# Kernel tuning notes

Measured on AMD Instinct MI355X. Metric: run time of the kernel, lower is better.

The kernel has to match this reference:

```python
import jax, jax.numpy as jnp
import numpy as np

N_NODES = 20000
N_EDGES = 320000
IN_CH = 512
HEADS = 4
OUT_CH = 128
NEG_SLOPE = 0.2  # PyG GATConv default leaky_relu slope


def setup_inputs() -> dict:
    key = jax.random.key(0)
    k1, k2, k3, k4, k5 = jax.random.split(key, 5)
    x = jax.random.normal(k1, (N_NODES, IN_CH), dtype=jnp.float32)
    edge_index = jax.random.randint(k2, (2, N_EDGES), 0, N_NODES, dtype=jnp.int64)
    # Learned parameters (glorot-ish scaling)
    W = jax.random.normal(k3, (IN_CH, HEADS * OUT_CH), dtype=jnp.float32) * np.float32(1.0 / np.sqrt(IN_CH))
    att_src = jax.random.normal(k4, (HEADS, OUT_CH), dtype=jnp.float32) * np.float32(0.1)
    att_dst = jax.random.normal(k5, (HEADS, OUT_CH), dtype=jnp.float32) * np.float32(0.1)
    bias = jnp.zeros((OUT_CH,), dtype=jnp.float32)
    return {"x": x, "W": W, "att_src": att_src, "att_dst": att_dst, "bias": bias, "edge_index": edge_index}


def reference(x, W, att_src, att_dst, bias, edge_index):
    N = x.shape[0]
    H, C = att_src.shape
    # add self-loops (PyG GATConv default add_self_loops=True)
    loop = jnp.arange(N, dtype=edge_index.dtype)
    ei = jnp.concatenate([edge_index, jnp.stack([loop, loop])], axis=1)
    src, dst = ei[0], ei[1]
    # linear projection: [N, H, C]
    xl = (x @ W).reshape(N, H, C)
    # per-node attention halves: [N, H]
    a_s = jnp.einsum('nhc,hc->nh', xl, att_src)
    a_d = jnp.einsum('nhc,hc->nh', xl, att_dst)
    # per-edge logits + segment softmax over incoming edges (grouped by dst)
    alpha = jax.nn.leaky_relu(a_s[src] + a_d[dst], negative_slope=NEG_SLOPE)  # [E, H]
    amax = jax.ops.segment_max(alpha, dst, num_segments=N)  # every node has a self-loop -> no empty segments
    ae = jnp.exp(alpha - amax[dst])
    denom = jax.ops.segment_sum(ae, dst, num_segments=N)
    alpha = ae / (denom[dst] + 1e-16)
    # weighted scatter-add of source features: [N, H, C]
    out = jax.ops.segment_sum(alpha[:, :, None] * xl[src], dst, num_segments=N)
    # concat=False -> mean over heads, then bias [C]
    out = out.mean(axis=1) + bias
    return jax.nn.elu(out)
```

## Files before the change

### kernel.cpp

```cpp
#include <hip/hip_runtime.h>
#include <math.h>

#define N_NODES 20000
#define N_PAD 20096
#define N_EDGES 320000
#define IN_CH 512
#define HEADS 4
#define OUT_CH 128
#define HC 512
#define NEG_SLOPE 0.2f

#define CVX_BLOCKS 5024
#define CVW_BLOCKS 64
#define CNT_BLOCKS 1250

#define GEMM_WGS 628
#define GEMM_XQ 78
#define GEMM_XR 4

typedef __attribute__((ext_vector_type(8))) short short8;
typedef __attribute__((ext_vector_type(4))) float float4v;

__device__ __forceinline__ int detect_is64(const int* __restrict__ ei32) {
    int is64 = 1;
    #pragma unroll
    for (int i = 0; i < 32; i++) is64 &= (ei32[2 * i + 1] == 0);
    return is64;
}

__device__ __forceinline__ int edge_at(const void* ei, int is64, long long idx) {
    return is64 ? (int)((const long long*)ei)[idx] : ((const int*)ei)[idx];
}

__device__ __forceinline__ unsigned short f2bf(float f) {
    union { float f; unsigned u; } v; v.f = f;
    unsigned r = v.u + 0x7fffu + ((v.u >> 16) & 1u);
    return (unsigned short)(r >> 16);
}

__device__ __forceinline__ void bf8_decode(uint4 r, float* f) {
    f[0] = __uint_as_float(r.x << 16); f[1] = __uint_as_float(r.x & 0xffff0000u);
    f[2] = __uint_as_float(r.y << 16); f[3] = __uint_as_float(r.y & 0xffff0000u);
    f[4] = __uint_as_float(r.z << 16); f[5] = __uint_as_float(r.z & 0xffff0000u);
    f[6] = __uint_as_float(r.w << 16); f[7] = __uint_as_float(r.w & 0xffff0000u);
}

__device__ __forceinline__ float leaky(float t) { return t > 0.f ? t : NEG_SLOPE * t; }

__device__ __forceinline__ float sel_head(float4 w, int hd) {
    float lo = (hd & 1) ? w.y : w.x;
    float hi = (hd & 1) ? w.w : w.z;
    return (hd & 2) ? hi : lo;
}

__global__ __launch_bounds__(256) void fusedA_kernel(const float* __restrict__ x,
                                                     const float* __restrict__ W,
                                                     unsigned short* __restrict__ xb,
                                                     unsigned short* __restrict__ Wt,
                                                     const void* __restrict__ ei,
                                                     int* __restrict__ counts,
                                                     int* __restrict__ epos) {
    __shared__ float tile[64][65];
    int b = blockIdx.x;
    if (b < CVX_BLOCKS) {
        size_t i = ((size_t)b * 256 + threadIdx.x) * 8;
        unsigned short o[8];
        if (i < (size_t)N_NODES * IN_CH) {
            float4 f0 = *(const float4*)&x[i];
            float4 f1 = *(const float4*)&x[i + 4];
            o[0] = f2bf(f0.x); o[1] = f2bf(f0.y); o[2] = f2bf(f0.z); o[3] = f2bf(f0.w);
            o[4] = f2bf(f1.x); o[5] = f2bf(f1.y); o[6] = f2bf(f1.z); o[7] = f2bf(f1.w);
        } else {
            for (int k = 0; k < 8; k++) o[k] = 0;
        }
        *(short8*)&xb[i] = *(short8*)o;
    } else if (b < CVX_BLOCKS + CVW_BLOCKS) {
        int idx = b - CVX_BLOCKS;
        int k0 = (idx & 7) * 64, n0 = (idx >> 3) * 64;
        int t = threadIdx.x, r = t >> 6, c = t & 63;
        for (int rr = r; rr < 64; rr += 4)
            tile[rr][c] = W[(size_t)(k0 + rr) * HC + n0 + c];
        __syncthreads();
        for (int rr = r; rr < 64; rr += 4)
            Wt[(size_t)(n0 + rr) * IN_CH + k0 + c] = f2bf(tile[c][rr]);
    } else {
        int is64 = detect_is64((const int*)ei);
        int e = (b - CVX_BLOCKS - CVW_BLOCKS) * 256 + threadIdx.x;
        if (e < N_EDGES) {
            int dst = edge_at(ei, is64, (long long)N_EDGES + e);
            int p = atomicAdd(&counts[dst], 1);
            epos[e] = p;
        }
    }
}

__global__ __launch_bounds__(256) void gemm_kernel(const unsigned short* __restrict__ A,
                                                   const unsigned short* __restrict__ Bt,
                                                   unsigned short* __restrict__ Cb,
                                                   const float* __restrict__ att_s,
                                                   const float* __restrict__ att_d,
                                                   float* __restrict__ a_s,
                                                   float* __restrict__ a_d) {
    __shared__ __align__(16) unsigned short As[2][128 * 32];
    __shared__ __align__(16) unsigned short Bs[2][128 * 32];
    __shared__ float ssum[128][2];
    __shared__ float dsum[128][2];

    const int bid = blockIdx.x;
    const int xcd = bid & 7, rank = bid >> 3;
    const int w = (xcd < GEMM_XR) ? xcd * (GEMM_XQ + 1) + rank
                                  : GEMM_XR * (GEMM_XQ + 1) + (xcd - GEMM_XR) * GEMM_XQ + rank;
    const int bm = (w >> 2) * 128;
    const int bn = (w & 3) * 128;

    const int t = threadIdx.x;
    const int wv = t >> 6, lane = t & 63;
    const int wm = wv & 1, wn = wv >> 1;
    const int lm = lane & 15, lk = lane >> 4;

    float4v acc[4][4];
    #pragma unroll
    for (int i = 0; i < 4; i++)
        #pragma unroll
        for (int j = 0; j < 4; j++) acc[i][j] = (float4v){0.f, 0.f, 0.f, 0.f};

    const int srow = t >> 2;
    const int sk   = ((t & 3) ^ ((t >> 3) & 3)) * 8;
    const int swr  = (lk ^ ((lm >> 1) & 3)) * 8;

#define GEMM_STAGE(buf, kof)                                                                  \
    {                                                                                         \
        _Pragma("unroll")                                                                     \
        for (int q = 0; q < 2; q++) {                                                         \
            const unsigned short* gA = A + (size_t)(bm + q * 64 + srow) * IN_CH + (kof) + sk; \
            const unsigned short* gB = Bt + (size_t)(bn + q * 64 + srow) * IN_CH + (kof) + sk;\
            __builtin_amdgcn_global_load_lds((const __attribute__((address_space(1))) void*)gA,\
                (__attribute__((address_space(3))) void*)&As[buf][q * 2048 + t * 8], 16, 0, 0);\
            __builtin_amdgcn_global_load_lds((const __attribute__((address_space(1))) void*)gB,\
                (__attribute__((address_space(3))) void*)&Bs[buf][q * 2048 + t * 8], 16, 0, 0);\
        }                                                                                     \
    }

    GEMM_STAGE(0, 0);
    int cur = 0;
    for (int kk = 0; kk < 16; ++kk) {
        if (kk < 15) {
            GEMM_STAGE(cur ^ 1, (kk + 1) * 32);
            asm volatile("s_waitcnt vmcnt(4)" ::: "memory");
        } else {
            asm volatile("s_waitcnt vmcnt(0)" ::: "memory");
        }
        __builtin_amdgcn_s_barrier();
        __builtin_amdgcn_sched_barrier(0);

        short8 af[4], bf[4];
        #pragma unroll
        for (int i = 0; i < 4; i++)
            af[i] = *(const short8*)&As[cur][(wm * 64 + i * 16 + lm) * 32 + swr];
        #pragma unroll
        for (int j = 0; j < 4; j++)
            bf[j] = *(const short8*)&Bs[cur][(wn * 64 + j * 16 + lm) * 32 + swr];
        #pragma unroll
        for (int i = 0; i < 4; i++)
            #pragma unroll
            for (int j = 0; j < 4; j++)
                acc[i][j] = __builtin_amdgcn_mfma_f32_16x16x32_bf16(af[i], bf[j], acc[i][j], 0, 0, 0);

        __builtin_amdgcn_sched_barrier(0);
        __builtin_amdgcn_s_barrier();
        cur ^= 1;
    }
#undef GEMM_STAGE

    #pragma unroll
    for (int i = 0; i < 4; i++) {
        #pragma unroll
        for (int r = 0; r < 4; r++) {
            int row = bm + wm * 64 + i * 16 + lk * 4 + r;
            if (row < N_NODES) {
                #pragma unroll
                for (int j = 0; j < 4; j++) {
                    int col = bn + wn * 64 + j * 16 + lm;
                    Cb[(size_t)row * HC + col] = f2bf(acc[i][j][r]);
                }
            }
        }
    }

    const int h = bn >> 7;
    float as_w[4], ad_w[4];
    #pragma unroll
    for (int j = 0; j < 4; j++) {
        int col = bn + wn * 64 + j * 16 + lm;
        as_w[j] = att_s[col];
        ad_w[j] = att_d[col];
    }
    float ps[4][4], pd[4][4];
    #pragma unroll
    for (int i = 0; i < 4; i++)
        #pragma unroll
        for (int r = 0; r < 4; r++) {
            float s = 0.f, d = 0.f;
            #pragma unroll
            for (int j = 0; j < 4; j++) { s += acc[i][j][r] * as_w[j]; d += acc[i][j][r] * ad_w[j]; }
            ps[i][r] = s; pd[i][r] = d;
        }
    #pragma unroll
    for (int off = 1; off < 16; off <<= 1) {
        #pragma unroll
        for (int i = 0; i < 4; i++)
            #pragma unroll
            for (int r = 0; r < 4; r++) {
                ps[i][r] += __shfl_xor(ps[i][r], off, 64);
                pd[i][r] += __shfl_xor(pd[i][r], off, 64);
            }
    }
    if (lm == 0) {
        #pragma unroll
        for (int i = 0; i < 4; i++)
            #pragma unroll
            for (int r = 0; r < 4; r++) {
                int rl = wm * 64 + i * 16 + lk * 4 + r;
                ssum[rl][wn] = ps[i][r];
                dsum[rl][wn] = pd[i][r];
            }
    }
    __syncthreads();
    if (t < 128) {
        int row = bm + t;
        if (row < N_NODES) {
            a_s[row * 4 + h] = ssum[t][0] + ssum[t][1];
            a_d[row * 4 + h] = dsum[t][0] + dsum[t][1];
        }
    }
}

__global__ __launch_bounds__(1024) void scan_kernel(const int* __restrict__ counts,
                                                    int* __restrict__ offsets) {
    const int CHUNK = 20;
    int tid = threadIdx.x;
    int base = tid * CHUNK;
    int c[CHUNK];
    #pragma unroll
    for (int k = 0; k < CHUNK; k++) {
        int i = base + k;
        c[k] = (i < N_NODES) ? counts[i] : 0;
    }
    int pre[CHUNK];
    int sum = 0;
    #pragma unroll
    for (int k = 0; k < CHUNK; k++) { pre[k] = sum; sum += c[k]; }

    int lane = tid & 63, wvv = tid >> 6;
    int s = sum;
    #pragma unroll
    for (int off = 1; off < 64; off <<= 1) {
        int u = __shfl_up(s, off, 64);
        if (lane >= off) s += u;
    }
    __shared__ int wsum[16];
    if (lane == 63) wsum[wvv] = s;
    __syncthreads();
    if (tid < 16) {
        int u = wsum[tid];
        #pragma unroll
        for (int off = 1; off < 16; off <<= 1) {
            int w = __shfl_up(u, off, 64);
            if (tid >= off) u += w;
        }
        wsum[tid] = u;
    }
    __syncthreads();
    int wbase = (wvv == 0) ? 0 : wsum[wvv - 1];
    int excl = wbase + s - sum;
    #pragma unroll
    for (int k = 0; k < CHUNK; k++) {
        int i = base + k;
        if (i < N_NODES) offsets[i] = excl + pre[k];
    }
    if (tid == 1023) offsets[N_NODES] = wbase + s;
}

__global__ __launch_bounds__(256) void scatterw_kernel(const void* __restrict__ ei,
                                                       const int* __restrict__ offsets,
                                                       const int* __restrict__ epos,
                                                       int* __restrict__ sorted_src,
                                                       const float* __restrict__ a_s,
                                                       const float* __restrict__ a_d,
                                                       float* __restrict__ edge_w) {
    int is64 = detect_is64((const int*)ei);
    int e = blockIdx.x * 256 + threadIdx.x;
    if (e < N_EDGES) {
        int dst = edge_at(ei, is64, (long long)N_EDGES + e);
        int src = edge_at(ei, is64, e);
        int pos = offsets[dst] + epos[e];
        sorted_src[pos] = src;
        float4 as4 = *(const float4*)&a_s[src * 4];
        float4 ad4 = *(const float4*)&a_d[dst * 4];
        float4 w;
        w.x = __expf(leaky(as4.x + ad4.x));
        w.y = __expf(leaky(as4.y + ad4.y));
        w.z = __expf(leaky(as4.z + ad4.z));
        w.w = __expf(leaky(as4.w + ad4.w));
        *(float4*)&edge_w[(size_t)pos * 4] = w;
    }
}

__global__ __launch_bounds__(256) void gather_kernel(const unsigned short* __restrict__ xlb,
                                                     const float* __restrict__ a_s,
                                                     const float* __restrict__ a_d,
                                                     const int* __restrict__ offsets,
                                                     const int* __restrict__ sorted_src,
                                                     const float* __restrict__ edge_w,
                                                     const float* __restrict__ bias,
                                                     float* __restrict__ out) {
    __shared__ float cl[3][64][9];
    int sub = threadIdx.x >> 6;
    int node = blockIdx.x;
    int lane = threadIdx.x & 63;
    int hd = lane >> 4;
    int beg = offsets[node], end = offsets[node + 1];

    const unsigned short* xrow = xlb + lane * 8;
    float acc[8] = {0, 0, 0, 0, 0, 0, 0, 0};
    float denom = 0.f;

    if (sub == 0) {
        float4 as4 = *(const float4*)&a_s[node * 4];
        float4 ad4 = *(const float4*)&a_d[node * 4];
        float4 ws;
        ws.x = __expf(leaky(as4.x + ad4.x));
        ws.y = __expf(leaky(as4.y + ad4.y));
        ws.z = __expf(leaky(as4.z + ad4.z));
        ws.w = __expf(leaky(as4.w + ad4.w));
        float w = sel_head(ws, hd);
        denom = w;
        uint4 r = *(const uint4*)(xrow + (size_t)node * HC);
        float f[8];
        bf8_decode(r, f);
        #pragma unroll
        for (int k = 0; k < 8; k++) acc[k] = w * f[k];
    }

    for (int c0 = beg + sub * 4; c0 < end; c0 += 16) {
        int n = end - c0;
        if (n >= 4) {
            int s0 = sorted_src[c0];
            int s1 = sorted_src[c0 + 1];
            int s2 = sorted_src[c0 + 2];
            int s3 = sorted_src[c0 + 3];
            uint4 r0 = *(const uint4*)(xrow + (size_t)s0 * HC);
            uint4 r1 = *(const uint4*)(xrow + (size_t)s1 * HC);
            uint4 r2 = *(const uint4*)(xrow + (size_t)s2 * HC);
            uint4 r3 = *(const uint4*)(xrow + (size_t)s3 * HC);
            float4 wa = *(const float4*)&edge_w[(size_t)c0 * 4];
            float4 wb = *(const float4*)&edge_w[(size_t)(c0 + 1) * 4];
            float4 wc = *(const float4*)&edge_w[(size_t)(c0 + 2) * 4];
            float4 wd = *(const float4*)&edge_w[(size_t)(c0 + 3) * 4];
            float w0 = sel_head(wa, hd), w1 = sel_head(wb, hd);
            float w2 = sel_head(wc, hd), w3 = sel_head(wd, hd);
            denom += (w0 + w1) + (w2 + w3);
            float f0[8], f1[8], f2[8], f3[8];
            bf8_decode(r0, f0);
            bf8_decode(r1, f1);
            bf8_decode(r2, f2);
            bf8_decode(r3, f3);
            #pragma unroll
            for (int k = 0; k < 8; k++)
                acc[k] += (w0 * f0[k] + w1 * f1[k]) + (w2 * f2[k] + w3 * f3[k]);
        } else {
            for (int j = 0; j < n; j++) {
                int s0 = sorted_src[c0 + j];
                uint4 r0 = *(const uint4*)(xrow + (size_t)s0 * HC);
                float4 wa = *(const float4*)&edge_w[(size_t)(c0 + j) * 4];
                float w0 = sel_head(wa, hd);
                denom += w0;
                float f0[8];
                bf8_decode(r0, f0);
                #pragma unroll
                for (int k = 0; k < 8; k++) acc[k] += w0 * f0[k];
            }
        }
    }

    if (sub != 0) {
        #pragma unroll
        for (int k = 0; k < 8; k++) cl[sub - 1][lane][k] = acc[k];
        cl[sub - 1][lane][8] = denom;
    }
    __syncthreads();
    if (sub == 0) {
        #pragma unroll
        for (int p = 0; p < 3; p++) {
            #pragma unroll
            for (int k = 0; k < 8; k++) acc[k] += cl[p][lane][k];
            denom += cl[p][lane][8];
        }

        float rd = 0.25f / (denom + 1e-16f);
        float v[8];
        #pragma unroll
        for (int k = 0; k < 8; k++) {
            float t = acc[k] * rd;
            t += __shfl_xor(t, 16, 64);
            t += __shfl_xor(t, 32, 64);
            v[k] = t;
        }
        if (hd == 0) {
            float4 b0 = *(const float4*)&bias[lane * 8];
            float4 b1 = *(const float4*)&bias[lane * 8 + 4];
            float o[8];
            o[0] = v[0] + b0.x; o[1] = v[1] + b0.y; o[2] = v[2] + b0.z; o[3] = v[3] + b0.w;
            o[4] = v[4] + b1.x; o[5] = v[5] + b1.y; o[6] = v[6] + b1.z; o[7] = v[7] + b1.w;
            #pragma unroll
            for (int k = 0; k < 8; k++) o[k] = o[k] > 0.f ? o[k] : expm1f(o[k]);
            *(float4*)&out[(size_t)node * OUT_CH + lane * 8]     = make_float4(o[0], o[1], o[2], o[3]);
            *(float4*)&out[(size_t)node * OUT_CH + lane * 8 + 4] = make_float4(o[4], o[5], o[6], o[7]);
        }
    }
}

extern "C" void kernel_launch(void* const* d_in, const int* in_sizes, int n_in,
                              void* d_out, int out_size, void* d_ws, size_t ws_size,
                              hipStream_t stream) {
    const float* x       = (const float*)d_in[0];
    const float* W       = (const float*)d_in[1];
    const float* att_src = (const float*)d_in[2];
    const float* att_dst = (const float*)d_in[3];
    const float* bias    = (const float*)d_in[4];
    const void*  ei      = d_in[5];
    float* out = (float*)d_out;

    char* ws = (char*)d_ws;
    size_t off = 0;
    unsigned short* xlb = (unsigned short*)(ws + off); off += (size_t)N_PAD * HC * sizeof(unsigned short);
    float* a_s     = (float*)(ws + off); off += (size_t)N_NODES * HEADS * sizeof(float);
    float* a_d     = (float*)(ws + off); off += (size_t)N_NODES * HEADS * sizeof(float);
    int* counts    = (int*)(ws + off);   off += (size_t)N_NODES * sizeof(int);
    int* offsets   = (int*)(ws + off);   off += (size_t)(N_NODES + 1) * sizeof(int);
    off = (off + 15) & ~(size_t)15;
    int* epos      = (int*)(ws + off);   off += (size_t)N_EDGES * sizeof(int);
    int* sorted_src = (int*)(ws + off);  off += (size_t)N_EDGES * sizeof(int);
    off = (off + 15) & ~(size_t)15;
    float* edge_w  = (float*)(ws + off); off += (size_t)N_EDGES * HEADS * sizeof(float);
    unsigned short* xb = (unsigned short*)(ws + off); off += (size_t)N_PAD * IN_CH * sizeof(unsigned short);
    unsigned short* Wt = (unsigned short*)(ws + off); off += (size_t)IN_CH * HC * sizeof(unsigned short);

    hipMemsetAsync(counts, 0, N_NODES * sizeof(int), stream);
    fusedA_kernel<<<CVX_BLOCKS + CVW_BLOCKS + CNT_BLOCKS, 256, 0, stream>>>(x, W, xb, Wt, ei, counts, epos);
    gemm_kernel<<<GEMM_WGS, 256, 0, stream>>>(xb, Wt, xlb, att_src, att_dst, a_s, a_d);
    scan_kernel<<<1, 1024, 0, stream>>>(counts, offsets);
    scatterw_kernel<<<(N_EDGES + 255) / 256, 256, 0, stream>>>(ei, offsets, epos, sorted_src, a_s, a_d, edge_w);
    gather_kernel<<<N_NODES, 256, 0, stream>>>(xlb, a_s, a_d, offsets, sorted_src, edge_w, bias, out);
}
```

Baseline: 214.3 us.

## Shrink GEMM tile to 64 rows with triple buffering; pack two nodes per gather block

```diff
diff --git a/kernel.cpp b/kernel.cpp
--- a/kernel.cpp
+++ b/kernel.cpp
@@ -14,9 +14,7 @@
 #define CVW_BLOCKS 64
 #define CNT_BLOCKS 1250
 
-#define GEMM_WGS 628
-#define GEMM_XQ 78
-#define GEMM_XR 4
+#define GEMM_WGS 1256
 
 typedef __attribute__((ext_vector_type(8))) short short8;
 typedef __attribute__((ext_vector_type(4))) float float4v;
@@ -101,16 +99,14 @@
                                                    const float* __restrict__ att_d,
                                                    float* __restrict__ a_s,
                                                    float* __restrict__ a_d) {
-    __shared__ __align__(16) unsigned short As[2][128 * 32];
-    __shared__ __align__(16) unsigned short Bs[2][128 * 32];
-    __shared__ float ssum[128][2];
-    __shared__ float dsum[128][2];
+    __shared__ __align__(16) unsigned short As[3][64 * 32];
+    __shared__ __align__(16) unsigned short Bs[3][128 * 32];
+    __shared__ float ssum[64][2];
+    __shared__ float dsum[64][2];
 
     const int bid = blockIdx.x;
-    const int xcd = bid & 7, rank = bid >> 3;
-    const int w = (xcd < GEMM_XR) ? xcd * (GEMM_XQ + 1) + rank
-                                  : GEMM_XR * (GEMM_XQ + 1) + (xcd - GEMM_XR) * GEMM_XQ + rank;
-    const int bm = (w >> 2) * 128;
+    const int w = (bid & 7) * 157 + (bid >> 3);
+    const int bm = (w >> 2) * 64;
     const int bn = (w & 3) * 128;
 
     const int t = threadIdx.x;
@@ -118,9 +114,9 @@
     const int wm = wv & 1, wn = wv >> 1;
     const int lm = lane & 15, lk = lane >> 4;
 
-    float4v acc[4][4];
-    #pragma unroll
-    for (int i = 0; i < 4; i++)
+    float4v acc[2][4];
+    #pragma unroll
+    for (int i = 0; i < 2; i++)
         #pragma unroll
         for (int j = 0; j < 4; j++) acc[i][j] = (float4v){0.f, 0.f, 0.f, 0.f};
 
@@ -128,55 +124,58 @@
     const int sk   = ((t & 3) ^ ((t >> 3) & 3)) * 8;
     const int swr  = (lk ^ ((lm >> 1) & 3)) * 8;
 
-#define GEMM_STAGE(buf, kof)                                                                  \
-    {                                                                                         \
-        _Pragma("unroll")                                                                     \
-        for (int q = 0; q < 2; q++) {                                                         \
-            const unsigned short* gA = A + (size_t)(bm + q * 64 + srow) * IN_CH + (kof) + sk; \
-            const unsigned short* gB = Bt + (size_t)(bn + q * 64 + srow) * IN_CH + (kof) + sk;\
-            __builtin_amdgcn_global_load_lds((const __attribute__((address_space(1))) void*)gA,\
-                (__attribute__((address_space(3))) void*)&As[buf][q * 2048 + t * 8], 16, 0, 0);\
+#define GEMM_STAGE(buf, kof)                                                                   \
+    {                                                                                          \
+        const unsigned short* gA = A + (size_t)(bm + srow) * IN_CH + (kof) + sk;               \
+        __builtin_amdgcn_global_load_lds((const __attribute__((address_space(1))) void*)gA,    \
+            (__attribute__((address_space(3))) void*)&As[buf][t * 8], 16, 0, 0);               \
+        _Pragma("unroll")                                                                      \
+        for (int q = 0; q < 2; q++) {                                                          \
+            const unsigned short* gB = Bt + (size_t)(bn + q * 64 + srow) * IN_CH + (kof) + sk; \
             __builtin_amdgcn_global_load_lds((const __attribute__((address_space(1))) void*)gB,\
                 (__attribute__((address_space(3))) void*)&Bs[buf][q * 2048 + t * 8], 16, 0, 0);\
-        }                                                                                     \
+        }                                                                                      \
     }
 
     GEMM_STAGE(0, 0);
-    int cur = 0;
+    GEMM_STAGE(1, 32);
+    #pragma unroll
     for (int kk = 0; kk < 16; ++kk) {
-        if (kk < 15) {
-            GEMM_STAGE(cur ^ 1, (kk + 1) * 32);
-            asm volatile("s_waitcnt vmcnt(4)" ::: "memory");
+        const int cur = kk % 3;
+        if (kk < 14) {
+            GEMM_STAGE((kk + 2) % 3, (kk + 2) * 32);
+            asm volatile("s_waitcnt vmcnt(6)" ::: "memory");
+        } else if (kk == 14) {
+            asm volatile("s_waitcnt vmcnt(3)" ::: "memory");
         } else {
             asm volatile("s_waitcnt vmcnt(0)" ::: "memory");
         }
         __builtin_amdgcn_s_barrier();
         __builtin_amdgcn_sched_barrier(0);
 
-        short8 af[4], bf[4];
-        #pragma unroll
-        for (int i = 0; i < 4; i++)
-            af[i] = *(const short8*)&As[cur][(wm * 64 + i * 16 + lm) * 32 + swr];
+        short8 af[2], bf[4];
+        #pragma unroll
+        for (int i = 0; i < 2; i++)
+            af[i] = *(const short8*)&As[cur][(wm * 32 + i * 16 + lm) * 32 + swr];
         #pragma unroll
         for (int j = 0; j < 4; j++)
             bf[j] = *(const short8*)&Bs[cur][(wn * 64 + j * 16 + lm) * 32 + swr];
         #pragma unroll
-        for (int i = 0; i < 4; i++)
+        for (int i = 0; i < 2; i++)
             #pragma unroll
             for (int j = 0; j < 4; j++)
                 acc[i][j] = __builtin_amdgcn_mfma_f32_16x16x32_bf16(af[i], bf[j], acc[i][j], 0, 0, 0);
 
         __builtin_amdgcn_sched_barrier(0);
         __builtin_amdgcn_s_barrier();
-        cur ^= 1;
     }
 #undef GEMM_STAGE
 
     #pragma unroll
-    for (int i = 0; i < 4; i++) {
+    for (int i = 0; i < 2; i++) {
         #pragma unroll
         for (int r = 0; r < 4; r++) {
-            int row = bm + wm * 64 + i * 16 + lk * 4 + r;
+            int row = bm + wm * 32 + i * 16 + lk * 4 + r;
             if (row < N_NODES) {
                 #pragma unroll
                 for (int j = 0; j < 4; j++) {
@@ -195,9 +194,9 @@
         as_w[j] = att_s[col];
         ad_w[j] = att_d[col];
     }
-    float ps[4][4], pd[4][4];
-    #pragma unroll
-    for (int i = 0; i < 4; i++)
+    float ps[2][4], pd[2][4];
+    #pragma unroll
+    for (int i = 0; i < 2; i++)
         #pragma unroll
         for (int r = 0; r < 4; r++) {
             float s = 0.f, d = 0.f;
@@ -208,7 +207,7 @@
     #pragma unroll
     for (int off = 1; off < 16; off <<= 1) {
         #pragma unroll
-        for (int i = 0; i < 4; i++)
+        for (int i = 0; i < 2; i++)
             #pragma unroll
             for (int r = 0; r < 4; r++) {
                 ps[i][r] += __shfl_xor(ps[i][r], off, 64);
@@ -217,16 +216,16 @@
     }
     if (lm == 0) {
         #pragma unroll
-        for (int i = 0; i < 4; i++)
+        for (int i = 0; i < 2; i++)
             #pragma unroll
             for (int r = 0; r < 4; r++) {
-                int rl = wm * 64 + i * 16 + lk * 4 + r;
+                int rl = wm * 32 + i * 16 + lk * 4 + r;
                 ssum[rl][wn] = ps[i][r];
                 dsum[rl][wn] = pd[i][r];
             }
     }
     __syncthreads();
-    if (t < 128) {
+    if (t < 64) {
         int row = bm + t;
         if (row < N_NODES) {
             a_s[row * 4 + h] = ssum[t][0] + ssum[t][1];
@@ -314,9 +313,11 @@
                                                      const float* __restrict__ edge_w,
                                                      const float* __restrict__ bias,
                                                      float* __restrict__ out) {
-    __shared__ float cl[3][64][9];
-    int sub = threadIdx.x >> 6;
-    int node = blockIdx.x;
+    __shared__ float cl[2][64][9];
+    int wv = threadIdx.x >> 6;
+    int nib = wv >> 1;
+    int sub = wv & 1;
+    int node = blockIdx.x * 2 + nib;
     int lane = threadIdx.x & 63;
     int hd = lane >> 4;
     int beg = offsets[node], end = offsets[node + 1];
@@ -324,6 +325,25 @@
     const unsigned short* xrow = xlb + lane * 8;
     float acc[8] = {0, 0, 0, 0, 0, 0, 0, 0};
     float denom = 0.f;
+
+    int c0 = beg + sub * 4;
+    int s0 = 0, s1 = 0, s2 = 0, s3 = 0;
+    float w0 = 0.f, w1 = 0.f, w2 = 0.f, w3 = 0.f;
+    if (c0 < end) {
+        int lim = end - 1;
+        int i1 = c0 + 1 > lim ? lim : c0 + 1;
+        int i2 = c0 + 2 > lim ? lim : c0 + 2;
+        int i3 = c0 + 3 > lim ? lim : c0 + 3;
+        s0 = sorted_src[c0]; s1 = sorted_src[i1]; s2 = sorted_src[i2]; s3 = sorted_src[i3];
+        float4 t0 = *(const float4*)&edge_w[(size_t)c0 * 4];
+        float4 t1 = *(const float4*)&edge_w[(size_t)i1 * 4];
+        float4 t2 = *(const float4*)&edge_w[(size_t)i2 * 4];
+        float4 t3 = *(const float4*)&edge_w[(size_t)i3 * 4];
+        w0 = sel_head(t0, hd);
+        w1 = (c0 + 1 < end) ? sel_head(t1, hd) : 0.f;
+        w2 = (c0 + 2 < end) ? sel_head(t2, hd) : 0.f;
+        w3 = (c0 + 3 < end) ? sel_head(t3, hd) : 0.f;
+    }
 
     if (sub == 0) {
         float4 as4 = *(const float4*)&a_s[node * 4];
@@ -342,60 +362,55 @@
         for (int k = 0; k < 8; k++) acc[k] = w * f[k];
     }
 
-    for (int c0 = beg + sub * 4; c0 < end; c0 += 16) {
-        int n = end - c0;
-        if (n >= 4) {
-            int s0 = sorted_src[c0];
-            int s1 = sorted_src[c0 + 1];
-            int s2 = sorted_src[c0 + 2];
-            int s3 = sorted_src[c0 + 3];
-            uint4 r0 = *(const uint4*)(xrow + (size_t)s0 * HC);
-            uint4 r1 = *(const uint4*)(xrow + (size_t)s1 * HC);
-            uint4 r2 = *(const uint4*)(xrow + (size_t)s2 * HC);
-            uint4 r3 = *(const uint4*)(xrow + (size_t)s3 * HC);
-            float4 wa = *(const float4*)&edge_w[(size_t)c0 * 4];
-            float4 wb = *(const float4*)&edge_w[(size_t)(c0 + 1) * 4];
-            float4 wc = *(const float4*)&edge_w[(size_t)(c0 + 2) * 4];
-            float4 wd = *(const float4*)&edge_w[(size_t)(c0 + 3) * 4];
-            float w0 = sel_head(wa, hd), w1 = sel_head(wb, hd);
-            float w2 = sel_head(wc, hd), w3 = sel_head(wd, hd);
-            denom += (w0 + w1) + (w2 + w3);
-            float f0[8], f1[8], f2[8], f3[8];
-            bf8_decode(r0, f0);
-            bf8_decode(r1, f1);
-            bf8_decode(r2, f2);
-            bf8_decode(r3, f3);
-            #pragma unroll
-            for (int k = 0; k < 8; k++)
-                acc[k] += (w0 * f0[k] + w1 * f1[k]) + (w2 * f2[k] + w3 * f3[k]);
-        } else {
-            for (int j = 0; j < n; j++) {
-                int s0 = sorted_src[c0 + j];
-                uint4 r0 = *(const uint4*)(xrow + (size_t)s0 * HC);
-                float4 wa = *(const float4*)&edge_w[(size_t)(c0 + j) * 4];
-                float w0 = sel_head(wa, hd);
-                denom += w0;
-                float f0[8];
-                bf8_decode(r0, f0);
-                #pragma unroll
-                for (int k = 0; k < 8; k++) acc[k] += w0 * f0[k];
-            }
-        }
-    }
-
-    if (sub != 0) {
-        #pragma unroll
-        for (int k = 0; k < 8; k++) cl[sub - 1][lane][k] = acc[k];
-        cl[sub - 1][lane][8] = denom;
+    for (; c0 < end; c0 += 8) {
+        uint4 r0 = *(const uint4*)(xrow + (size_t)s0 * HC);
+        uint4 r1 = *(const uint4*)(xrow + (size_t)s1 * HC);
+        uint4 r2 = *(const uint4*)(xrow + (size_t)s2 * HC);
+        uint4 r3 = *(const uint4*)(xrow + (size_t)s3 * HC);
+
+        int c1 = c0 + 8;
+        int n0 = 0, n1 = 0, n2 = 0, n3 = 0;
+        float v0 = 0.f, v1 = 0.f, v2 = 0.f, v3 = 0.f;
+        if (c1 < end) {
+            int lim = end - 1;
+            int i1 = c1 + 1 > lim ? lim : c1 + 1;
+            int i2 = c1 + 2 > lim ? lim : c1 + 2;
+            int i3 = c1 + 3 > lim ? lim : c1 + 3;
+            n0 = sorted_src[c1]; n1 = sorted_src[i1]; n2 = sorted_src[i2]; n3 = sorted_src[i3];
+            float4 t0 = *(const float4*)&edge_w[(size_t)c1 * 4];
+            float4 t1 = *(const float4*)&edge_w[(size_t)i1 * 4];
+            float4 t2 = *(const float4*)&edge_w[(size_t)i2 * 4];
+            float4 t3 = *(const float4*)&edge_w[(size_t)i3 * 4];
+            v0 = sel_head(t0, hd);
+            v1 = (c1 + 1 < end) ? sel_head(t1, hd) : 0.f;
+            v2 = (c1 + 2 < end) ? sel_head(t2, hd) : 0.f;
+            v3 = (c1 + 3 < end) ? sel_head(t3, hd) : 0.f;
+        }
+
+        denom += (w0 + w1) + (w2 + w3);
+        float f0[8], f1[8], f2[8], f3[8];
+        bf8_decode(r0, f0);
+        bf8_decode(r1, f1);
+        bf8_decode(r2, f2);
+        bf8_decode(r3, f3);
+        #pragma unroll
+        for (int k = 0; k < 8; k++)
+            acc[k] += (w0 * f0[k] + w1 * f1[k]) + (w2 * f2[k] + w3 * f3[k]);
+
+        s0 = n0; s1 = n1; s2 = n2; s3 = n3;
+        w0 = v0; w1 = v1; w2 = v2; w3 = v3;
+    }
+
+    if (sub == 1) {
+        #pragma unroll
+        for (int k = 0; k < 8; k++) cl[nib][lane][k] = acc[k];
+        cl[nib][lane][8] = denom;
     }
     __syncthreads();
     if (sub == 0) {
         #pragma unroll
-        for (int p = 0; p < 3; p++) {
-            #pragma unroll
-            for (int k = 0; k < 8; k++) acc[k] += cl[p][lane][k];
-            denom += cl[p][lane][8];
-        }
+        for (int k = 0; k < 8; k++) acc[k] += cl[nib][lane][k];
+        denom += cl[nib][lane][8];
 
         float rd = 0.25f / (denom + 1e-16f);
         float v[8];
@@ -451,5 +466,5 @@
     gemm_kernel<<<GEMM_WGS, 256, 0, stream>>>(xb, Wt, xlb, att_src, att_dst, a_s, a_d);
     scan_kernel<<<1, 1024, 0, stream>>>(counts, offsets);
     scatterw_kernel<<<(N_EDGES + 255) / 256, 256, 0, stream>>>(ei, offsets, epos, sorted_src, a_s, a_d, edge_w);
-    gather_kernel<<<N_NODES, 256, 0, stream>>>(xlb, a_s, a_d, offsets, sorted_src, edge_w, bias, out);
-}
+    gather_kernel<<<N_NODES / 2, 256, 0, stream>>>(xlb, a_s, a_d, offsets, sorted_src, edge_w, bias, out);
+}
```

After: 209.7 us. 1.02x faster.
